# Performance work log

Hardware: AMD Instinct MI355X
Metric: run time of the kernel (lower is better)

The kernel has to match this reference:

```python
import jax, jax.numpy as jnp
import numpy as np
import math

B, S, DIM = 2, 2048, 2048
H, KV, HD = 16, 1, 128  # query heads, kv heads, head dim


def setup_inputs() -> dict:
    key = jax.random.key(0)
    ks = jax.random.split(key, 6)
    std = 0.02
    return {
        "hidden_states": jax.random.normal(ks[0], (B, S, DIM), jnp.float32),
        "attention_mask": jnp.zeros((B, 1, S, S), jnp.float32),
        "wq": jax.random.normal(ks[1], (DIM, H * HD), jnp.float32) * std,
        "bq": jnp.zeros((H * HD,), jnp.float32),
        "wk": jax.random.normal(ks[2], (DIM, KV * HD), jnp.float32) * std,
        "bk": jnp.zeros((KV * HD,), jnp.float32),
        "wv": jax.random.normal(ks[3], (DIM, KV * HD), jnp.float32) * std,
        "bv": jnp.zeros((KV * HD,), jnp.float32),
        "wo": jax.random.normal(ks[4], (H * HD, DIM), jnp.float32) * std,
        "bo": jnp.zeros((DIM,), jnp.float32),
    }


def reference(hidden_states, attention_mask, wq, bq, wk, bk, wv, bv, wo, bo):
    b, s, _ = hidden_states.shape
    q = (hidden_states @ wq + bq).reshape(b, s, H, HD)
    k = (hidden_states @ wk + bk).reshape(b, s, KV, HD)
    v = (hidden_states @ wv + bv).reshape(b, s, KV, HD)
    # [b, h, s, d]
    q = jnp.transpose(q, (0, 2, 1, 3))
    k = jnp.transpose(k, (0, 2, 1, 3))
    v = jnp.transpose(v, (0, 2, 1, 3))
    # broadcast shared KV heads to all query heads (num_kv_heads < num_query_heads)
    repeats = H // KV
    k = jnp.repeat(k, repeats, axis=1)
    v = jnp.repeat(v, repeats, axis=1)
    scores = jnp.einsum('bhqd,bhkd->bhqk', q, k) / math.sqrt(HD)
    scores = scores + attention_mask
    weights = jax.nn.softmax(scores, axis=-1)
    attn = jnp.einsum('bhqk,bhkd->bhqd', weights, v)
    attn = jnp.transpose(attn, (0, 2, 1, 3)).reshape(b, s, H * HD)
    return attn @ wo + bo
```

## Files before the change

### kernel.cpp

```cpp
#include <hip/hip_runtime.h>
#include <hip/hip_bf16.h>
#include <stdint.h>

#define S_LEN 2048
#define DIMSZ 2048
#define NH    16
#define HD    128
#define NQK   2176
#define NQKV  2304

typedef short  bf16x8  __attribute__((ext_vector_type(8)));
typedef float  floatx4 __attribute__((ext_vector_type(4)));
typedef float  floatx16 __attribute__((ext_vector_type(16)));
typedef int    intx4   __attribute__((ext_vector_type(4)));
typedef unsigned short u16;

#define mfma32 __builtin_amdgcn_mfma_f32_32x32x16_bf16
#define LOG2E 1.4426950408889634f

__device__ __forceinline__ u16 f2bf(float x) {
  unsigned int u = __builtin_bit_cast(unsigned int, x);
  u = (u + 0x7FFFu + ((u >> 16) & 1u)) >> 16;
  return (u16)u;
}

__device__ __forceinline__ int cvtpk(float lo, float hi) {
  int r;
  asm("v_cvt_pk_bf16_f32 %0, %1, %2" : "=v"(r) : "v"(lo), "v"(hi));
  return r;
}

#if __has_builtin(__builtin_amdgcn_exp2f)
__device__ __forceinline__ float fexp2(float x) { return __builtin_amdgcn_exp2f(x); }
#else
__device__ __forceinline__ float fexp2(float x) { return exp2f(x); }
#endif

#if __has_builtin(__builtin_amdgcn_permlane32_swap)
__device__ __forceinline__ void half_swap(int& a, int& b) {
  auto r = __builtin_amdgcn_permlane32_swap(a, b, false, false);
  a = (int)r[0]; b = (int)r[1];
}
__device__ __forceinline__ float red_max32(float x) {
  int xi = __builtin_bit_cast(int, x);
  auto r = __builtin_amdgcn_permlane32_swap(xi, xi, false, false);
  return fmaxf(__builtin_bit_cast(float, (int)r[0]), __builtin_bit_cast(float, (int)r[1]));
}
__device__ __forceinline__ float red_add32(float x) {
  int xi = __builtin_bit_cast(int, x);
  auto r = __builtin_amdgcn_permlane32_swap(xi, xi, false, false);
  return __builtin_bit_cast(float, (int)r[0]) + __builtin_bit_cast(float, (int)r[1]);
}
#else
__device__ __forceinline__ void half_swap(int& a, int& b) {
  int as = __shfl_xor(a, 32);
  int bs = __shfl_xor(b, 32);
  int lane = threadIdx.x & 63;
  int na = (lane < 32) ? a : bs;
  int nb = (lane < 32) ? as : b;
  a = na; b = nb;
}
__device__ __forceinline__ float red_max32(float x) { return fmaxf(x, __shfl_xor(x, 32)); }
__device__ __forceinline__ float red_add32(float x) { return x + __shfl_xor(x, 32); }
#endif

__device__ __forceinline__ void gload16(const void* g, void* l) {
  __builtin_amdgcn_global_load_lds(
      reinterpret_cast<const __attribute__((address_space(1))) void*>(reinterpret_cast<uintptr_t>(g)),
      reinterpret_cast<__attribute__((address_space(3))) void*>(reinterpret_cast<uintptr_t>(l)),
      16, 0, 0);
}

__global__ void k_cvt_bf16(const float* __restrict__ in, u16* __restrict__ out, int n4) {
  int i = blockIdx.x * blockDim.x + threadIdx.x;
  if (i < n4) {
    float4 v = ((const float4*)in)[i];
    ushort4 o;
    o.x = f2bf(v.x); o.y = f2bf(v.y); o.z = f2bf(v.z); o.w = f2bf(v.w);
    ((ushort4*)out)[i] = o;
  }
}

__global__ void k_transpose_bf16(const float* __restrict__ in, u16* __restrict__ out,
                                 int K, int N, int rowOff) {
  __shared__ float t[64][65];
  int c0 = blockIdx.x * 64;
  int r0 = blockIdx.y * 64;
  int tid = threadIdx.x;
  int lr = tid >> 6;
  int lc = tid & 63;
#pragma unroll
  for (int i = 0; i < 16; ++i) {
    int r = lr + i * 4;
    t[r][lc] = in[(size_t)(r0 + r) * N + c0 + lc];
  }
  __syncthreads();
#pragma unroll
  for (int i = 0; i < 16; ++i) {
    int r = lr + i * 4;
    out[(size_t)(rowOff + c0 + r) * K + r0 + lc] = f2bf(t[lc][r]);
  }
}

__global__ void k_bias_concat(const float* __restrict__ bq, const float* __restrict__ bk,
                              const float* __restrict__ bv, float* __restrict__ out) {
  int i = blockIdx.x * 256 + threadIdx.x;
  if (i < NQKV) out[i] = (i < 2048) ? bq[i] : (i < NQK ? bk[i - 2048] : bv[i - NQK]);
}

__device__ __forceinline__ void stage_tile(const u16* __restrict__ G, int ldg, int row0, int kt,
                                           u16* lbase, int wid, int lane) {
#pragma unroll
  for (int i = 0; i < 4; ++i) {
    int c   = (wid * 4 + i) * 64 + lane;
    int row = c >> 3, cin = c & 7;
    int cs  = cin ^ (row & 7);
    const u16* g = G + (size_t)(row0 + row) * ldg + kt * 64 + cs * 8;
    gload16(g, (char*)lbase + (wid * 4 + i) * 1024);
  }
}

template <int OMODE>
__global__ __launch_bounds__(256)
void k_gemm(const u16* __restrict__ A, const u16* __restrict__ Bt,
            const float* __restrict__ bias, void* __restrict__ Cout,
            u16* __restrict__ vt, int M, int N, int K) {
  __shared__ u16 lA[2][128 * 64];
  __shared__ u16 lB[2][128 * 64];
  const int tid = threadIdx.x, lane = tid & 63, wid = tid >> 6;
  const int wm = wid >> 1, wn = wid & 1;
  const int tm = blockIdx.x, tn = blockIdx.y;
  const int nk = K >> 6;

  stage_tile(A, K, tm * 128, 0, lA[0], wid, lane);
  stage_tile(Bt, K, tn * 128, 0, lB[0], wid, lane);
  __syncthreads();

  floatx4 acc[4][4] = {};
  int buf = 0;
  for (int kt = 0; kt < nk; ++kt) {
    if (kt + 1 < nk) {
      stage_tile(A, K, tm * 128, kt + 1, lA[buf ^ 1], wid, lane);
      stage_tile(Bt, K, tn * 128, kt + 1, lB[buf ^ 1], wid, lane);
    }
    const char* pa = (const char*)&lA[buf][0];
    const char* pb = (const char*)&lB[buf][0];
#pragma unroll
    for (int kk = 0; kk < 2; ++kk) {
      bf16x8 af[4], bfr[4];
      int gch = kk * 4 + (lane >> 4);
#pragma unroll
      for (int f = 0; f < 4; ++f) {
        int ra = wm * 64 + f * 16 + (lane & 15);
        af[f]  = *(const bf16x8*)(pa + ra * 128 + ((gch ^ (ra & 7)) << 4));
        int rb = wn * 64 + f * 16 + (lane & 15);
        bfr[f] = *(const bf16x8*)(pb + rb * 128 + ((gch ^ (rb & 7)) << 4));
      }
      __builtin_amdgcn_s_setprio(1);
#pragma unroll
      for (int fm = 0; fm < 4; ++fm)
#pragma unroll
        for (int fn = 0; fn < 4; ++fn)
          acc[fm][fn] = __builtin_amdgcn_mfma_f32_16x16x32_bf16(af[fm], bfr[fn], acc[fm][fn], 0, 0, 0);
      __builtin_amdgcn_s_setprio(0);
    }
    __syncthreads();
    buf ^= 1;
  }

#pragma unroll
  for (int fm = 0; fm < 4; ++fm)
#pragma unroll
    for (int fn = 0; fn < 4; ++fn)
#pragma unroll
      for (int r = 0; r < 4; ++r) {
        int rowg = tm * 128 + wm * 64 + fm * 16 + (lane >> 4) * 4 + r;
        int colg = tn * 128 + wn * 64 + fn * 16 + (lane & 15);
        float v = acc[fm][fn][r] + bias[colg];
        if constexpr (OMODE == 1) {
          ((float*)Cout)[(size_t)rowg * N + colg] = v;
        } else {
          if (colg < NQK) {
            ((u16*)Cout)[(size_t)rowg * N + colg] = f2bf(v);
          } else {
            int d = colg - NQK;
            int bg = rowg >> 11, s = rowg & 2047;
            vt[((size_t)bg * HD + d) * S_LEN + s] = f2bf(v);
          }
        }
      }
}

__device__ __forceinline__ void stage_kv(const u16* __restrict__ qkv, const u16* __restrict__ vt,
                                         int b, int kt, u16* lK, u16* lV, int wid, int lane) {
#pragma unroll
  for (int i = 0; i < 2; ++i) {
    int seg = wid * 2 + i;
    {
      int r = seg * 4 + (lane >> 4), cin = lane & 15;
      const u16* g = qkv + (size_t)(b * S_LEN + kt * 64 + r) * NQKV + 2048 + ((cin ^ (r & 7)) * 8);
      gload16(g, (char*)lK + seg * 1024);
    }
    {
      int r = seg * 8 + (lane >> 3), cin = lane & 7;
      const u16* g = vt + ((size_t)b * HD + r) * S_LEN + kt * 64 + ((cin ^ (r & 7)) * 8);
      gload16(g, (char*)lV + seg * 1024);
    }
  }
}

__global__ __launch_bounds__(512)
void k_attn(const u16* __restrict__ qkv, const u16* __restrict__ vt,
            const float* __restrict__ mask, u16* __restrict__ attn) {
  __shared__ __align__(16) u16   lK[2][64 * 128];
  __shared__ __align__(16) u16   lV[2][128 * 64];
  __shared__ __align__(16) float lM[2][32 * 64];
  const int tid = threadIdx.x, lane = tid & 63, wid = tid >> 6;
  const int qt = blockIdx.x, hg = blockIdx.y, b = blockIdx.z;
  const int h = hg * 8 + wid;
  const int q = lane & 31, h5 = lane >> 5;
  const float c_sl2 = 0.08838834764831845f * LOG2E;

  bf16x8 qf[8];
  const size_t qrow = (size_t)(b * S_LEN + qt * 32 + q);
#pragma unroll
  for (int cs = 0; cs < 8; ++cs)
    qf[cs] = *(const bf16x8*)(qkv + qrow * NQKV + h * HD + cs * 16 + h5 * 8);

  float m_ = -1e30f, l_ = 0.f;
  floatx16 acco[4] = {};

  const int mq = tid >> 4, mc = tid & 15;
  const float* mrow = mask + (size_t)b * S_LEN * S_LEN + (size_t)(qt * 32 + mq) * S_LEN + mc * 4;

  stage_kv(qkv, vt, b, 0, lK[0], lV[0], wid, lane);
  floatx4 mreg = *(const floatx4*)(mrow);
  *(floatx4*)((char*)&lM[0][0] + mq * 256 + ((mc ^ (mq & 7)) << 4)) = mreg * LOG2E;
  __syncthreads();

  int buf = 0;
  for (int kt = 0; kt < S_LEN / 64; ++kt) {
    if (kt + 1 < S_LEN / 64) {
      stage_kv(qkv, vt, b, kt + 1, lK[buf ^ 1], lV[buf ^ 1], wid, lane);
      mreg = *(const floatx4*)(mrow + (size_t)(kt + 1) * 64);
    }

    floatx16 accs0 = {}, accs1 = {};
    const char* pK = (const char*)&lK[buf][0];
    __builtin_amdgcn_s_setprio(1);
#pragma unroll
    for (int cs = 0; cs < 8; ++cs) {
      int c = cs * 2 + h5;
      bf16x8 kf0 = *(const bf16x8*)(pK + q * 256 + ((c ^ (q & 7)) << 4));
      bf16x8 kf1 = *(const bf16x8*)(pK + (32 + q) * 256 + ((c ^ (q & 7)) << 4));
      accs0 = mfma32(kf0, qf[cs], accs0, 0, 0, 0);
      accs1 = mfma32(kf1, qf[cs], accs1, 0, 0, 0);
    }
    __builtin_amdgcn_s_setprio(0);

    float pr[32];
    float rowm = -1e30f;
    const char* pM = (const char*)&lM[buf][0];
#pragma unroll
    for (int kb = 0; kb < 2; ++kb)
#pragma unroll
      for (int rg = 0; rg < 4; ++rg) {
        int c = kb * 8 + rg * 2 + h5;
        floatx4 m4 = *(const floatx4*)(pM + q * 256 + ((c ^ (q & 7)) << 4));
#pragma unroll
        for (int t = 0; t < 4; ++t) {
          float sv = (kb ? accs1[rg * 4 + t] : accs0[rg * 4 + t]) * c_sl2 + m4[t];
          pr[kb * 16 + rg * 4 + t] = sv;
          rowm = fmaxf(rowm, sv);
        }
      }
    rowm = red_max32(rowm);
    if (__any(rowm > m_ + 11.5415603f)) {
      float mn = fmaxf(m_, rowm);
      float al = fexp2(m_ - mn);
      m_ = mn;
      l_ *= al;
#pragma unroll
      for (int dt = 0; dt < 4; ++dt) acco[dt] *= al;
    }
    float sum = 0.f;
#pragma unroll
    for (int j = 0; j < 32; ++j) {
      float e = fexp2(pr[j] - m_);
      pr[j] = e;
      sum += e;
    }
    l_ += red_add32(sum);

    bf16x8 pf[4];
#pragma unroll
    for (int kb = 0; kb < 2; ++kb)
#pragma unroll
      for (int s = 0; s < 2; ++s) {
        int base = kb * 16 + s * 8;
        int A0 = cvtpk(pr[base + 0], pr[base + 1]);
        int A1 = cvtpk(pr[base + 2], pr[base + 3]);
        int B0 = cvtpk(pr[base + 4], pr[base + 5]);
        int B1 = cvtpk(pr[base + 6], pr[base + 7]);
        half_swap(A0, B0);
        half_swap(A1, B1);
        intx4 w;
        w[0] = A0; w[1] = A1; w[2] = B0; w[3] = B1;
        pf[kb * 2 + s] = __builtin_bit_cast(bf16x8, w);
      }

    const char* pV = (const char*)&lV[buf][0];
    __builtin_amdgcn_s_setprio(1);
#pragma unroll
    for (int dt = 0; dt < 4; ++dt) {
      int rd = dt * 32 + q;
#pragma unroll
      for (int ks = 0; ks < 4; ++ks) {
        int c = ks * 2 + h5;
        bf16x8 vf = *(const bf16x8*)(pV + rd * 128 + ((c ^ (q & 7)) << 4));
        acco[dt] = mfma32(vf, pf[ks], acco[dt], 0, 0, 0);
      }
    }
    __builtin_amdgcn_s_setprio(0);

    if (kt + 1 < S_LEN / 64)
      *(floatx4*)((char*)&lM[buf ^ 1][0] + mq * 256 + ((mc ^ (mq & 7)) << 4)) = mreg * LOG2E;
    __syncthreads();
    buf ^= 1;
  }

  float inv = 1.0f / l_;
  u16* obase = attn + qrow * DIMSZ + h * HD;
#pragma unroll
  for (int dt = 0; dt < 4; ++dt)
#pragma unroll
    for (int rg = 0; rg < 4; ++rg) {
      int d0 = dt * 32 + rg * 8 + h5 * 4;
      ushort4 st;
      st.x = f2bf(acco[dt][rg * 4 + 0] * inv);
      st.y = f2bf(acco[dt][rg * 4 + 1] * inv);
      st.z = f2bf(acco[dt][rg * 4 + 2] * inv);
      st.w = f2bf(acco[dt][rg * 4 + 3] * inv);
      *(ushort4*)(obase + d0) = st;
    }
}

extern "C" void kernel_launch(void* const* d_in, const int* in_sizes, int n_in,
                              void* d_out, int out_size, void* d_ws, size_t ws_size,
                              hipStream_t stream) {
  const float* hidden = (const float*)d_in[0];
  const float* mask   = (const float*)d_in[1];
  const float* wq = (const float*)d_in[2];
  const float* bq = (const float*)d_in[3];
  const float* wk = (const float*)d_in[4];
  const float* bk = (const float*)d_in[5];
  const float* wv = (const float*)d_in[6];
  const float* bv = (const float*)d_in[7];
  const float* wo = (const float*)d_in[8];
  const float* bo = (const float*)d_in[9];
  float* out = (float*)d_out;

  char* ws = (char*)d_ws;
  u16*   hb    = (u16*)(ws);
  u16*   wqkvT = (u16*)(ws + 16777216);
  u16*   woT   = (u16*)(ws + 26214400);
  float* bqkv  = (float*)(ws + 34603008);
  u16*   qkv   = (u16*)(ws + 34612224);
  u16*   vt    = (u16*)(ws + 53486592);
  u16*   attn  = (u16*)(ws + 54535168);

  k_cvt_bf16<<<dim3(8192), dim3(256), 0, stream>>>(hidden, hb, 4096 * 2048 / 4);
  k_transpose_bf16<<<dim3(32, 32), dim3(256), 0, stream>>>(wq, wqkvT, 2048, 2048, 0);
  k_transpose_bf16<<<dim3(2, 32),  dim3(256), 0, stream>>>(wk, wqkvT, 2048, 128, 2048);
  k_transpose_bf16<<<dim3(2, 32),  dim3(256), 0, stream>>>(wv, wqkvT, 2048, 128, NQK);
  k_transpose_bf16<<<dim3(32, 32), dim3(256), 0, stream>>>(wo, woT, 2048, 2048, 0);
  k_bias_concat<<<dim3(9), dim3(256), 0, stream>>>(bq, bk, bv, bqkv);

  k_gemm<0><<<dim3(32, 18), dim3(256), 0, stream>>>(hb, wqkvT, bqkv, (void*)qkv, vt, 4096, NQKV, 2048);
  k_attn<<<dim3(64, 2, 2), dim3(512), 0, stream>>>(qkv, vt, mask, attn);
  k_gemm<1><<<dim3(32, 16), dim3(256), 0, stream>>>(attn, woT, bo, (void*)out, (u16*)nullptr, 4096, 2048, 2048);
}
```

Baseline: 204.7 us.

## Split attention KV range in two halves and merge partial outputs

The attention kernel now splits the key sequence into two halves across extra blocks, which doubles the grid so more of the GPU's compute units get work. Each half writes a bf16 partial output plus a log-sum-exp value into scratch space. The log-sum-exp goes into the now-unused V columns of the qkv buffer, and the partial outputs go into the freed hidden-state buffer. A new merge kernel combines the two halves. The mask is also kept in LDS as bf16 rather than fp32, and the row max and sum reductions are split into four independent chains for more instruction-level parallelism. The cost is an extra kernel launch, extra global memory traffic for the partial outputs, and a small precision loss from rounding the mask and partials to bf16.

```diff
diff --git a/kernel.cpp b/kernel.cpp
--- a/kernel.cpp
+++ b/kernel.cpp
@@ -8,11 +8,13 @@
 #define HD    128
 #define NQK   2176
 #define NQKV  2304
+#define NT    (S_LEN / 64)
 
 typedef short  bf16x8  __attribute__((ext_vector_type(8)));
 typedef float  floatx4 __attribute__((ext_vector_type(4)));
 typedef float  floatx16 __attribute__((ext_vector_type(16)));
 typedef int    intx4   __attribute__((ext_vector_type(4)));
+typedef int    intx2   __attribute__((ext_vector_type(2)));
 typedef unsigned short u16;
 
 #define mfma32 __builtin_amdgcn_mfma_f32_32x32x16_bf16
@@ -22,6 +24,9 @@
   unsigned int u = __builtin_bit_cast(unsigned int, x);
   u = (u + 0x7FFFu + ((u >> 16) & 1u)) >> 16;
   return (u16)u;
+}
+__device__ __forceinline__ float bf2f(unsigned int bits) {
+  return __builtin_bit_cast(float, bits << 16);
 }
 
 __device__ __forceinline__ int cvtpk(float lo, float hi) {
@@ -209,17 +214,26 @@
   }
 }
 
+__device__ __forceinline__ void mask_write(u16* lMb, int mq, int mc, floatx4 m) {
+  intx2 w;
+  w[0] = cvtpk(m[0] * LOG2E, m[1] * LOG2E);
+  w[1] = cvtpk(m[2] * LOG2E, m[3] * LOG2E);
+  *(intx2*)((char*)lMb + mq * 128 + ((mc ^ (mq & 15)) << 3)) = w;
+}
+
 __global__ __launch_bounds__(512)
 void k_attn(const u16* __restrict__ qkv, const u16* __restrict__ vt,
-            const float* __restrict__ mask, u16* __restrict__ attn) {
-  __shared__ __align__(16) u16   lK[2][64 * 128];
-  __shared__ __align__(16) u16   lV[2][128 * 64];
-  __shared__ __align__(16) float lM[2][32 * 64];
+            const float* __restrict__ mask, u16* __restrict__ pO0,
+            u16* __restrict__ pO1, float* __restrict__ qkvf) {
+  __shared__ __align__(16) u16 lK[2][64 * 128];
+  __shared__ __align__(16) u16 lV[2][128 * 64];
+  __shared__ __align__(16) u16 lMb[2][32 * 64];
   const int tid = threadIdx.x, lane = tid & 63, wid = tid >> 6;
-  const int qt = blockIdx.x, hg = blockIdx.y, b = blockIdx.z;
+  const int qt = blockIdx.x, hg = blockIdx.y & 1, kh = blockIdx.y >> 1, b = blockIdx.z;
   const int h = hg * 8 + wid;
   const int q = lane & 31, h5 = lane >> 5;
   const float c_sl2 = 0.08838834764831845f * LOG2E;
+  const int kt0 = kh * (NT / 2), kt1 = kt0 + (NT / 2);
 
   bf16x8 qf[8];
   const size_t qrow = (size_t)(b * S_LEN + qt * 32 + q);
@@ -233,14 +247,14 @@
   const int mq = tid >> 4, mc = tid & 15;
   const float* mrow = mask + (size_t)b * S_LEN * S_LEN + (size_t)(qt * 32 + mq) * S_LEN + mc * 4;
 
-  stage_kv(qkv, vt, b, 0, lK[0], lV[0], wid, lane);
-  floatx4 mreg = *(const floatx4*)(mrow);
-  *(floatx4*)((char*)&lM[0][0] + mq * 256 + ((mc ^ (mq & 7)) << 4)) = mreg * LOG2E;
+  stage_kv(qkv, vt, b, kt0, lK[0], lV[0], wid, lane);
+  floatx4 mreg = *(const floatx4*)(mrow + (size_t)kt0 * 64);
+  mask_write(&lMb[0][0], mq, mc, mreg);
   __syncthreads();
 
   int buf = 0;
-  for (int kt = 0; kt < S_LEN / 64; ++kt) {
-    if (kt + 1 < S_LEN / 64) {
+  for (int kt = kt0; kt < kt1; ++kt) {
+    if (kt + 1 < kt1) {
       stage_kv(qkv, vt, b, kt + 1, lK[buf ^ 1], lV[buf ^ 1], wid, lane);
       mreg = *(const floatx4*)(mrow + (size_t)(kt + 1) * 64);
     }
@@ -259,22 +273,25 @@
     __builtin_amdgcn_s_setprio(0);
 
     float pr[32];
-    float rowm = -1e30f;
-    const char* pM = (const char*)&lM[buf][0];
+    float pm0 = -1e30f, pm1 = -1e30f, pm2 = -1e30f, pm3 = -1e30f;
+    const char* pM = (const char*)&lMb[buf][0];
 #pragma unroll
     for (int kb = 0; kb < 2; ++kb)
 #pragma unroll
       for (int rg = 0; rg < 4; ++rg) {
         int c = kb * 8 + rg * 2 + h5;
-        floatx4 m4 = *(const floatx4*)(pM + q * 256 + ((c ^ (q & 7)) << 4));
-#pragma unroll
-        for (int t = 0; t < 4; ++t) {
-          float sv = (kb ? accs1[rg * 4 + t] : accs0[rg * 4 + t]) * c_sl2 + m4[t];
-          pr[kb * 16 + rg * 4 + t] = sv;
-          rowm = fmaxf(rowm, sv);
-        }
+        ushort4 mu = *(const ushort4*)(pM + q * 128 + ((c ^ (q & 15)) << 3));
+        float s0 = (kb ? accs1[rg * 4 + 0] : accs0[rg * 4 + 0]) * c_sl2 + bf2f(mu.x);
+        float s1 = (kb ? accs1[rg * 4 + 1] : accs0[rg * 4 + 1]) * c_sl2 + bf2f(mu.y);
+        float s2 = (kb ? accs1[rg * 4 + 2] : accs0[rg * 4 + 2]) * c_sl2 + bf2f(mu.z);
+        float s3 = (kb ? accs1[rg * 4 + 3] : accs0[rg * 4 + 3]) * c_sl2 + bf2f(mu.w);
+        pr[kb * 16 + rg * 4 + 0] = s0; pm0 = fmaxf(pm0, s0);
+        pr[kb * 16 + rg * 4 + 1] = s1; pm1 = fmaxf(pm1, s1);
+        pr[kb * 16 + rg * 4 + 2] = s2; pm2 = fmaxf(pm2, s2);
+        pr[kb * 16 + rg * 4 + 3] = s3; pm3 = fmaxf(pm3, s3);
       }
-    rowm = red_max32(rowm);
+    float rowm = red_max32(fmaxf(fmaxf(pm0, pm1), fmaxf(pm2, pm3)));
+
     if (__any(rowm > m_ + 11.5415603f)) {
       float mn = fmaxf(m_, rowm);
       float al = fexp2(m_ - mn);
@@ -283,14 +300,15 @@
 #pragma unroll
       for (int dt = 0; dt < 4; ++dt) acco[dt] *= al;
     }
-    float sum = 0.f;
-#pragma unroll
-    for (int j = 0; j < 32; ++j) {
-      float e = fexp2(pr[j] - m_);
-      pr[j] = e;
-      sum += e;
-    }
-    l_ += red_add32(sum);
+    float ps0 = 0.f, ps1 = 0.f, ps2 = 0.f, ps3 = 0.f;
+#pragma unroll
+    for (int j = 0; j < 32; j += 4) {
+      float e0 = fexp2(pr[j + 0] - m_); pr[j + 0] = e0; ps0 += e0;
+      float e1 = fexp2(pr[j + 1] - m_); pr[j + 1] = e1; ps1 += e1;
+      float e2 = fexp2(pr[j + 2] - m_); pr[j + 2] = e2; ps2 += e2;
+      float e3 = fexp2(pr[j + 3] - m_); pr[j + 3] = e3; ps3 += e3;
+    }
+    l_ += red_add32((ps0 + ps1) + (ps2 + ps3));
 
     bf16x8 pf[4];
 #pragma unroll
@@ -323,14 +341,14 @@
     }
     __builtin_amdgcn_s_setprio(0);
 
-    if (kt + 1 < S_LEN / 64)
-      *(floatx4*)((char*)&lM[buf ^ 1][0] + mq * 256 + ((mc ^ (mq & 7)) << 4)) = mreg * LOG2E;
+    if (kt + 1 < kt1)
+      mask_write(&lMb[buf ^ 1][0], mq, mc, mreg);
     __syncthreads();
     buf ^= 1;
   }
 
   float inv = 1.0f / l_;
-  u16* obase = attn + qrow * DIMSZ + h * HD;
+  u16* obase = (kh ? pO1 : pO0) + qrow * DIMSZ + h * HD;
 #pragma unroll
   for (int dt = 0; dt < 4; ++dt)
 #pragma unroll
@@ -343,6 +361,43 @@
       st.w = f2bf(acco[dt][rg * 4 + 3] * inv);
       *(ushort4*)(obase + d0) = st;
     }
+  if (h5 == 0) {
+    float mtil = m_ + __log2f(l_);
+    int j = kh * 65536 + (b * NH + h) * S_LEN + qt * 32 + q;
+    qkvf[(size_t)(j >> 6) * (NQKV / 2) + (NQK / 2) + (j & 63)] = mtil;
+  }
+}
+
+__global__ __launch_bounds__(256)
+void k_merge(const u16* __restrict__ p0, u16* __restrict__ p1,
+             const float* __restrict__ qkvf) {
+  int idx = blockIdx.x * 256 + threadIdx.x;
+  size_t gi = (size_t)idx * 8;
+  int row = (int)(gi >> 11);
+  int col = (int)(gi & 2047);
+  int h = col >> 7;
+  int b = row >> 11, sq = row & 2047;
+  int j0 = (b * NH + h) * S_LEN + sq;
+  int j1 = 65536 + j0;
+  float mt0 = qkvf[(size_t)(j0 >> 6) * (NQKV / 2) + (NQK / 2) + (j0 & 63)];
+  float mt1 = qkvf[(size_t)(j1 >> 6) * (NQKV / 2) + (NQK / 2) + (j1 & 63)];
+  float M = fmaxf(mt0, mt1);
+  float w0 = fexp2(mt0 - M), w1 = fexp2(mt1 - M);
+  float inv = 1.0f / (w0 + w1);
+  w0 *= inv; w1 *= inv;
+  intx4 a = *(const intx4*)(p0 + gi);
+  intx4 c = *(const intx4*)(p1 + gi);
+  intx4 o;
+#pragma unroll
+  for (int i = 0; i < 4; ++i) {
+    unsigned int wa = (unsigned int)a[i], wc = (unsigned int)c[i];
+    float lo = w0 * __builtin_bit_cast(float, wa << 16) +
+               w1 * __builtin_bit_cast(float, wc << 16);
+    float hi = w0 * __builtin_bit_cast(float, wa & 0xFFFF0000u) +
+               w1 * __builtin_bit_cast(float, wc & 0xFFFF0000u);
+    o[i] = cvtpk(lo, hi);
+  }
+  *(intx4*)(p1 + gi) = o;
 }
 
 extern "C" void kernel_launch(void* const* d_in, const int* in_sizes, int n_in,
@@ -377,6 +432,7 @@
   k_bias_concat<<<dim3(9), dim3(256), 0, stream>>>(bq, bk, bv, bqkv);
 
   k_gemm<0><<<dim3(32, 18), dim3(256), 0, stream>>>(hb, wqkvT, bqkv, (void*)qkv, vt, 4096, NQKV, 2048);
-  k_attn<<<dim3(64, 2, 2), dim3(512), 0, stream>>>(qkv, vt, mask, attn);
+  k_attn<<<dim3(64, 4, 2), dim3(512), 0, stream>>>(qkv, vt, mask, hb, attn, (float*)qkv);
+  k_merge<<<dim3(4096), dim3(256), 0, stream>>>(hb, attn, (const float*)qkv);
   k_gemm<1><<<dim3(32, 16), dim3(256), 0, stream>>>(attn, woT, bo, (void*)out, (u16*)nullptr, 4096, 2048, 2048);
 }
```

Measured after the change: 221.1 us. 8.0% more time.
